# Kernel optimization log

Hardware: AMD Instinct MI355X
Metric: run time of the kernel (lower is better)

Reference implementation:

```python
import jax, jax.numpy as jnp
import numpy as np

N_NODES = 20000


def _gcn_norm(edge_index, n):
    src, dst = edge_index[0], edge_index[1]
    # degree of A + I (self-loops), all edge weights 1
    deg = jax.ops.segment_sum(jnp.ones(src.shape[0], jnp.float32), dst, num_segments=n) + 1.0
    dinv = jax.lax.rsqrt(deg)
    norm = dinv[src] * dinv[dst]          # [E]
    self_norm = dinv * dinv               # [N] self-loop coefficient = 1/deg
    return src, dst, norm, self_norm


def _gcn_layer(x, W, b, src, dst, norm, self_norm):
    # x: [B, N, Fin]; W: [Fin, Fout]
    h = jnp.einsum('bnf,fo->bno', x, W)   # transform first (PyG GCNConv order)
    msg = h[:, src, :] * norm[None, :, None]                      # [B, E, Fout]
    agg = jax.vmap(lambda m: jax.ops.segment_sum(m, dst, num_segments=x.shape[1]))(msg)
    agg = agg + h * self_norm[None, :, None]                      # self-loop term
    return agg + b


def setup_inputs() -> dict:
    key = jax.random.key(0)
    ks = jax.random.split(key, 8)
    B, N, Fin, H, O, E = 2, N_NODES, 256, 256, 64, 320000
    s = lambda f: 1.0 / np.sqrt(f)
    return {
        'x': jax.random.normal(ks[0], (B, N, Fin), jnp.float32),
        'W1': jax.random.normal(ks[1], (Fin, H), jnp.float32) * s(Fin),
        'b1': jnp.zeros((H,), jnp.float32),
        'W2': jax.random.normal(ks[2], (H, H), jnp.float32) * s(H),
        'b2': jnp.zeros((H,), jnp.float32),
        'Wfc': jax.random.normal(ks[3], (H, O), jnp.float32) * s(H),
        'bfc': jnp.zeros((O,), jnp.float32),
        'edge_index': jax.random.randint(ks[4], (2, E), 0, N, jnp.int64),
    }


def reference(x, W1, b1, W2, b2, Wfc, bfc, edge_index):
    src, dst, norm, self_norm = _gcn_norm(edge_index, x.shape[1])
    h = jax.nn.relu(_gcn_layer(x, W1, b1, src, dst, norm, self_norm))
    h = jax.nn.relu(_gcn_layer(h, W2, b2, src, dst, norm, self_norm))
    pooled = jnp.mean(h, axis=1)          # mean over nodes -> [B, H]
    return pooled @ Wfc + bfc             # [B, O]
```

## Files before the change

### kernel.cpp

```cpp
#include <hip/hip_runtime.h>

#define NNODES 20000
#define BATCH  2
#define FEAT   256
#define OOUT   64
#define PBLK   200
#define MROWS  40000
#define NPB    20096
#define H8ROWS 40192

typedef short  bhalf8 __attribute__((ext_vector_type(8)));
typedef float  floatx4 __attribute__((ext_vector_type(4)));
typedef float  floatx2 __attribute__((ext_vector_type(2)));

__device__ __forceinline__ float bf2f(unsigned short u) {
  return __uint_as_float(((unsigned int)u) << 16);
}
__device__ __forceinline__ unsigned short f2bf(float f) {
  unsigned int u = __float_as_uint(f);
  return (unsigned short)((u + 0x7fffu + ((u >> 16) & 1u)) >> 16);
}
__device__ __forceinline__ unsigned int pack4_fp8(float a, float b, float c, float d) {
  int p = __builtin_amdgcn_cvt_pk_fp8_f32(a, b, 0, false);
  p = __builtin_amdgcn_cvt_pk_fp8_f32(c, d, p, true);
  return (unsigned int)p;
}

__global__ __launch_bounds__(256) void prep_kernel(const float* __restrict__ W1,
                                                   const float* __restrict__ W2,
                                                   unsigned short* __restrict__ w1hi,
                                                   unsigned short* __restrict__ w1lo,
                                                   unsigned short* __restrict__ w2hi,
                                                   unsigned short* __restrict__ w2lo,
                                                   const int* __restrict__ raw, int E,
                                                   int* __restrict__ flag,
                                                   int* __restrict__ cnt,
                                                   int* __restrict__ fill) {
  int bid = blockIdx.x, tid = threadIdx.x;
  int idx = bid * 256 + tid;
  int which = idx >> 16, loc = idx & 65535;
  const float* W = which ? W2 : W1;
  unsigned short* Whi = which ? w2hi : w1hi;
  unsigned short* Wlo = which ? w2lo : w1lo;
  int k = loc >> 8, n = loc & 255;
  float w = W[loc];
  unsigned short hi = f2bf(w);
  unsigned short lo = f2bf(w - bf2f(hi));
  int g = n >> 4, ln = n & 15;
  int ks = k >> 5, ch = (k >> 3) & 3, j = k & 7;
  int addr = ((ks * 16 + g) * 64 + ch * 16 + ln) * 8 + j;
  Whi[addr] = hi;
  Wlo[addr] = lo;
  if (idx < NNODES) { cnt[idx] = 0; fill[idx] = 0; }
  if (bid == 511) {
    __shared__ int any;
    if (tid == 0) any = 0;
    __syncthreads();
    int nchk = E < 2048 ? E : 2048;
    for (int i = tid; i < nchk; i += 256)
      if (raw[2 * i + 1] != 0) any = 1;
    __syncthreads();
    if (tid == 0) *flag = any;
  }
}

__global__ void convert_count_kernel(const int* __restrict__ raw, const int* __restrict__ flag,
                                     int* __restrict__ s32, int* __restrict__ d32,
                                     int* __restrict__ cnt, int E) {
  int e = blockIdx.x * blockDim.x + threadIdx.x;
  if (e >= E) return;
  int s, d;
  if (*flag) { s = raw[e];     d = raw[E + e]; }
  else       { s = raw[2 * e]; d = raw[2 * (E + e)]; }
  s32[e] = s; d32[e] = d;
  atomicAdd(&cnt[d], 1);
}

__global__ __launch_bounds__(1024) void scan_dinv_kernel(const int* __restrict__ cnt,
                                                         int* __restrict__ row_start,
                                                         float* __restrict__ dinv, int n) {
  __shared__ int wsum[16];
  __shared__ int carry_s;
  int tid = threadIdx.x, lane = tid & 63, wv = tid >> 6;
  if (tid == 0) carry_s = 0;
  __syncthreads();
  for (int base = 0; base < n; base += 1024) {
    int v = (base + tid < n) ? cnt[base + tid] : 0;
    if (base + tid < n) dinv[base + tid] = 1.0f / sqrtf((float)(v + 1));
    int x = v;
#pragma unroll
    for (int off = 1; off < 64; off <<= 1) {
      int t = __shfl_up(x, off);
      if (lane >= off) x += t;
    }
    if (lane == 63) wsum[wv] = x;
    __syncthreads();
    int carry = carry_s;
    if (wv == 0) {
      int s = (lane < 16) ? wsum[lane] : 0;
#pragma unroll
      for (int off = 1; off < 16; off <<= 1) {
        int t = __shfl_up(s, off);
        if (lane >= off) s += t;
      }
      if (lane < 16) wsum[lane] = s;
    }
    __syncthreads();
    int woff = wv ? wsum[wv - 1] : 0;
    int total = wsum[15];
    if (base + tid < n) row_start[base + tid] = carry + woff + x - v;
    __syncthreads();
    if (tid == 0) carry_s = carry + total;
  }
  if (tid == 0) row_start[n] = carry_s;
}

__global__ void scatter_kernel(const int* __restrict__ s32, const int* __restrict__ d32,
                               const int* __restrict__ row_start, int* __restrict__ fill,
                               const float* __restrict__ dinv,
                               int* __restrict__ csr_src, float* __restrict__ csr_norm, int E) {
  int e = blockIdx.x * blockDim.x + threadIdx.x;
  if (e >= E) return;
  int s = s32[e], d = d32[e];
  int p = row_start[d] + atomicAdd(&fill[d], 1);
  csr_src[p] = s;
  csr_norm[p] = dinv[s] * dinv[d];
}

template <int AFP32>
__global__ __launch_bounds__(256) void gemm_mfma(const void* __restrict__ Av,
                                                 const unsigned short* __restrict__ Whi,
                                                 const unsigned short* __restrict__ Wlo,
                                                 unsigned int* __restrict__ C) {
  __shared__ unsigned short lds[2][8192];
  int bid = blockIdx.x;
  int tile = bid >> 1, half = bid & 1;
  int b = tile >= 157 ? 1 : 0;
  int nbase = (tile - b * 157) * 128;
  int tid = threadIdx.x, lane = tid & 63, wv = tid >> 6;
  int kc = (lane >> 4) * 8;

  const float* Af          = (const float*)Av;
  const unsigned short* Ab = (const unsigned short*)Av;

  int nn[2], mr[2];
#pragma unroll
  for (int t = 0; t < 2; ++t) {
    int nl = nbase + wv * 32 + t * 16 + (lane & 15);
    nn[t] = nl;
    int ncl = nl > NNODES - 1 ? NNODES - 1 : nl;
    mr[t] = b * NNODES + ncl;
  }

  floatx4 acc[2][8];
#pragma unroll
  for (int t = 0; t < 2; ++t)
#pragma unroll
    for (int g = 0; g < 8; ++g) acc[t][g] = (floatx4)(0.0f);

  bhalf8 st[4];
  auto stage_load = [&](int ks) {
#pragma unroll
    for (int i2 = 0; i2 < 4; ++i2) {
      int u = i2 * 256 + tid;
      int hl = u >> 9, g = (u >> 6) & 7, l = u & 63;
      const unsigned short* Wp = hl ? Wlo : Whi;
      st[i2] = *(const bhalf8*)&Wp[((size_t)(ks * 16 + half * 8 + g) * 64 + l) * 8];
    }
  };
  auto stage_write = [&](int buf) {
#pragma unroll
    for (int i2 = 0; i2 < 4; ++i2) {
      int u = i2 * 256 + tid;
      *(bhalf8*)&lds[buf][(size_t)u * 8] = st[i2];
    }
  };
  auto load_a = [&](int ks, bhalf8 (&a)[2]) {
#pragma unroll
    for (int t = 0; t < 2; ++t) {
      if (AFP32) {
        const float* p = &Af[(size_t)mr[t] * FEAT + ks * 32 + kc];
        float4 u = *(const float4*)p;
        float4 v = *(const float4*)(p + 4);
        a[t][0] = (short)f2bf(u.x); a[t][1] = (short)f2bf(u.y);
        a[t][2] = (short)f2bf(u.z); a[t][3] = (short)f2bf(u.w);
        a[t][4] = (short)f2bf(v.x); a[t][5] = (short)f2bf(v.y);
        a[t][6] = (short)f2bf(v.z); a[t][7] = (short)f2bf(v.w);
      } else {
        a[t] = *(const bhalf8*)&Ab[(size_t)mr[t] * FEAT + ks * 32 + kc];
      }
    }
  };
  auto step = [&](int buf, bhalf8 (&a)[2]) {
#pragma unroll
    for (int g = 0; g < 8; ++g) {
      bhalf8 bh = *(const bhalf8*)&lds[buf][((size_t)g * 64 + lane) * 8];
      bhalf8 bl = *(const bhalf8*)&lds[buf][((size_t)(512 + g * 64) + lane) * 8];
#pragma unroll
      for (int t = 0; t < 2; ++t)
        acc[t][g] = __builtin_amdgcn_mfma_f32_16x16x32_bf16(bh, a[t], acc[t][g], 0, 0, 0);
#pragma unroll
      for (int t = 0; t < 2; ++t)
        acc[t][g] = __builtin_amdgcn_mfma_f32_16x16x32_bf16(bl, a[t], acc[t][g], 0, 0, 0);
    }
  };

  stage_load(0);
  stage_write(0);
  __syncthreads();
  bhalf8 aC[2];
  load_a(0, aC);
  int cur = 0;
#pragma unroll
  for (int ks = 0; ks < 8; ++ks) {
    bhalf8 aN[2];
    if (ks < 7) {
      stage_load(ks + 1);
      load_a(ks + 1, aN);
    }
    step(cur, aC);
    if (ks < 7) {
      stage_write(cur ^ 1);
      __syncthreads();
      aC[0] = aN[0]; aC[1] = aN[1];
    }
    cur ^= 1;
  }

  int nc = (lane >> 4) * 4;
#pragma unroll
  for (int t = 0; t < 2; ++t) {
    size_t r = (size_t)nn[t] * 2 + b;
#pragma unroll
    for (int g = 0; g < 8; ++g) {
      int col = (half * 8 + g) * 16 + nc;
      C[r * 64 + (col >> 2)] =
          pack4_fp8(acc[t][g][0], acc[t][g][1], acc[t][g][2], acc[t][g][3]);
    }
  }
}

__global__ __launch_bounds__(128) void agg_kernel(const uint4* __restrict__ h8,
                                                  const int* __restrict__ row_start,
                                                  const int* __restrict__ csr_src,
                                                  const float* __restrict__ csr_norm,
                                                  const float* __restrict__ dinv,
                                                  const float* __restrict__ bias,
                                                  unsigned short* __restrict__ out) {
  int n = blockIdx.x;
  int tid = threadIdx.x;
  int wave = tid >> 6, lane = tid & 63;
  int q = (wave << 1) | (lane >> 5);
  int cl = lane & 31;

  float a[16];
#pragma unroll
  for (int j = 0; j < 16; ++j) a[j] = 0.0f;

  auto dec_fma = [&](uint4 m, float w) {
    unsigned int mm[4] = {m.x, m.y, m.z, m.w};
#pragma unroll
    for (int j = 0; j < 4; ++j) {
      floatx2 lo = __builtin_amdgcn_cvt_pk_f32_fp8((int)mm[j], false);
      floatx2 hi = __builtin_amdgcn_cvt_pk_f32_fp8((int)mm[j], true);
      a[j * 4 + 0] = fmaf(w, lo[0], a[j * 4 + 0]);
      a[j * 4 + 1] = fmaf(w, lo[1], a[j * 4 + 1]);
      a[j * 4 + 2] = fmaf(w, hi[0], a[j * 4 + 2]);
      a[j * 4 + 3] = fmaf(w, hi[1], a[j * 4 + 3]);
    }
  };

  float di = dinv[n];
  if (q == 0) dec_fma(h8[(size_t)n * 32 + cl], di * di);

  int s0 = row_start[n], s1 = row_start[n + 1];
  int i = s0 + q;
  for (; i + 4 < s1; i += 8) {
    int sa = csr_src[i], sb = csr_src[i + 4];
    float wa = csr_norm[i], wb = csr_norm[i + 4];
    uint4 ma = h8[(size_t)sa * 32 + cl];
    uint4 mb = h8[(size_t)sb * 32 + cl];
    dec_fma(ma, wa);
    dec_fma(mb, wb);
  }
  if (i < s1) dec_fma(h8[(size_t)csr_src[i] * 32 + cl], csr_norm[i]);

#pragma unroll
  for (int j = 0; j < 16; ++j) a[j] += __shfl_xor(a[j], 32);

  __shared__ float red[32][17];
  if (wave == 1 && lane < 32) {
#pragma unroll
    for (int j = 0; j < 16; ++j) red[lane][j] = a[j];
  }
  __syncthreads();
  if (wave == 0 && lane < 32) {
    int b = cl >> 4;
    int c = (cl & 15) * 16;
#pragma unroll
    for (int j = 0; j < 16; ++j) a[j] += red[lane][j];
    unsigned short o[16];
#pragma unroll
    for (int j = 0; j < 16; ++j)
      o[j] = f2bf(fmaxf(a[j] + bias[c + j], 0.0f));
    unsigned short* dst = &out[((size_t)b * NNODES + n) * FEAT + c];
    *(uint4*)dst = *(uint4*)&o[0];
    *(uint4*)(dst + 8) = *(uint4*)&o[8];
  }
}

__global__ __launch_bounds__(256) void pool_partial(const unsigned short* __restrict__ h2,
                                                    float* __restrict__ partials) {
  int blk = blockIdx.x;
  int c = threadIdx.x;
  int chunk = NNODES / PBLK;
  int n0 = blk * chunk;
  float s0 = 0.f, s1 = 0.f;
  for (int n = n0; n < n0 + chunk; ++n) {
    s0 += bf2f(h2[((size_t)0 * NNODES + n) * FEAT + c]);
    s1 += bf2f(h2[((size_t)1 * NNODES + n) * FEAT + c]);
  }
  partials[(blk * 2 + 0) * FEAT + c] = s0;
  partials[(blk * 2 + 1) * FEAT + c] = s1;
}

__global__ __launch_bounds__(256) void pool_fc(const float* __restrict__ partials,
                                               const float* __restrict__ Wfc, const float* __restrict__ bfc,
                                               float* __restrict__ out) {
  __shared__ float pooled[BATCH][FEAT];
  int t = threadIdx.x;
  float s0 = 0.f, s1 = 0.f;
  for (int p = 0; p < PBLK; ++p) {
    s0 += partials[(p * 2 + 0) * FEAT + t];
    s1 += partials[(p * 2 + 1) * FEAT + t];
  }
  pooled[0][t] = s0 / (float)NNODES;
  pooled[1][t] = s1 / (float)NNODES;
  __syncthreads();
  if (t < BATCH * OOUT) {
    int b = t >> 6, o = t & 63;
    float acc = bfc[o];
    for (int c2 = 0; c2 < FEAT; ++c2)
      acc = fmaf(pooled[b][c2], Wfc[c2 * OOUT + o], acc);
    out[b * OOUT + o] = acc;
  }
}

extern "C" void kernel_launch(void* const* d_in, const int* in_sizes, int n_in,
                              void* d_out, int out_size, void* d_ws, size_t ws_size,
                              hipStream_t stream) {
  const float* x    = (const float*)d_in[0];
  const float* W1   = (const float*)d_in[1];
  const float* b1   = (const float*)d_in[2];
  const float* W2   = (const float*)d_in[3];
  const float* b2   = (const float*)d_in[4];
  const float* Wfc  = (const float*)d_in[5];
  const float* bfc  = (const float*)d_in[6];
  const int*   eraw = (const int*)d_in[7];
  int E = in_sizes[7] / 2;
  float* out = (float*)d_out;

  char* ws = (char*)d_ws;
  size_t off = 0;
  auto alloc = [&](size_t elems4B) -> void* {
    void* p = ws + off * 4;
    off += (elems4B + 3) & ~(size_t)3;
    return p;
  };
  int*   flag      = (int*)alloc(4);
  int*   s32       = (int*)alloc(E);
  int*   d32       = (int*)alloc(E);
  int*   cnt       = (int*)alloc(NNODES);
  float* dinv      = (float*)alloc(NNODES);
  int*   row_start = (int*)alloc(NNODES + 1);
  int*   fill      = (int*)alloc(NNODES);
  int*   csr_src   = (int*)alloc(E);
  float* csr_norm  = (float*)alloc(E);
  unsigned short* w1hi = (unsigned short*)alloc(65536 / 2);
  unsigned short* w1lo = (unsigned short*)alloc(65536 / 2);
  unsigned short* w2hi = (unsigned short*)alloc(65536 / 2);
  unsigned short* w2lo = (unsigned short*)alloc(65536 / 2);
  unsigned int*   h8   = (unsigned int*)alloc((size_t)H8ROWS * 64);
  unsigned short* a1   = (unsigned short*)alloc((size_t)MROWS * FEAT / 2);
  float* partials  = (float*)alloc((size_t)PBLK * BATCH * FEAT);

  int eg = (E + 255) / 256;
  prep_kernel<<<512, 256, 0, stream>>>(W1, W2, w1hi, w1lo, w2hi, w2lo, eraw, E, flag, cnt, fill);
  convert_count_kernel<<<eg, 256, 0, stream>>>(eraw, flag, s32, d32, cnt, E);
  scan_dinv_kernel<<<1, 1024, 0, stream>>>(cnt, row_start, dinv, NNODES);
  scatter_kernel<<<eg, 256, 0, stream>>>(s32, d32, row_start, fill, dinv, csr_src, csr_norm, E);

  gemm_mfma<1><<<628, 256, 0, stream>>>(x, w1hi, w1lo, h8);
  agg_kernel<<<NNODES, 128, 0, stream>>>((const uint4*)h8, row_start, csr_src, csr_norm, dinv, b1, a1);
  gemm_mfma<0><<<628, 256, 0, stream>>>(a1, w2hi, w2lo, h8);
  agg_kernel<<<NNODES, 128, 0, stream>>>((const uint4*)h8, row_start, csr_src, csr_norm, dinv, b2, a1);
  pool_partial<<<PBLK, 256, 0, stream>>>(a1, partials);
  pool_fc<<<1, 256, 0, stream>>>(partials, Wfc, bfc, out);
}
```

Measured before the change: 188.9 us.

## Parallelize CSR scan, fuse layer-2 aggregation with pooling, remap GEMM blocks

Replaces the single-block serial scan with a 20-block chunked scan whose chunk offsets are added via atomics. It also drops the intermediate s32/d32 edge copies by re-reading the raw edge index in the scatter kernel. The second aggregation is fused with ReLU and mean pooling, so the layer-2 activations are never written out, and a 512-thread FC kernel reduces the per-block partials. The GEMM block index is remapped so both column halves of neighbouring tiles run close together, which should improve L2 reuse, at the cost of 12 idle padding blocks. The risk is a persistent-style agg2 loop with fewer blocks and two barriers per node.

```diff
diff --git a/kernel.cpp b/kernel.cpp
--- a/kernel.cpp
+++ b/kernel.cpp
@@ -4,10 +4,11 @@
 #define BATCH  2
 #define FEAT   256
 #define OOUT   64
-#define PBLK   200
 #define MROWS  40000
 #define NPB    20096
 #define H8ROWS 40192
+#define NCHUNK 20
+#define NB2    1280
 
 typedef short  bhalf8 __attribute__((ext_vector_type(8)));
 typedef float  floatx4 __attribute__((ext_vector_type(4)));
@@ -35,7 +36,8 @@
                                                    const int* __restrict__ raw, int E,
                                                    int* __restrict__ flag,
                                                    int* __restrict__ cnt,
-                                                   int* __restrict__ fill) {
+                                                   int* __restrict__ fill,
+                                                   int* __restrict__ chunkOff) {
   int bid = blockIdx.x, tid = threadIdx.x;
   int idx = bid * 256 + tid;
   int which = idx >> 16, loc = idx & 65535;
@@ -52,6 +54,7 @@
   Whi[addr] = hi;
   Wlo[addr] = lo;
   if (idx < NNODES) { cnt[idx] = 0; fill[idx] = 0; }
+  if (idx < NCHUNK) chunkOff[idx] = 0;
   if (bid == 511) {
     __shared__ int any;
     if (tid == 0) any = 0;
@@ -64,65 +67,61 @@
   }
 }
 
-__global__ void convert_count_kernel(const int* __restrict__ raw, const int* __restrict__ flag,
-                                     int* __restrict__ s32, int* __restrict__ d32,
-                                     int* __restrict__ cnt, int E) {
+__global__ void count_kernel(const int* __restrict__ raw, const int* __restrict__ flag,
+                             int* __restrict__ cnt, int E) {
+  int e = blockIdx.x * blockDim.x + threadIdx.x;
+  if (e >= E) return;
+  int d = (*flag) ? raw[E + e] : raw[2 * (E + e)];
+  atomicAdd(&cnt[d], 1);
+}
+
+__global__ __launch_bounds__(256) void scan_a_kernel(const int* __restrict__ cnt,
+                                                     int* __restrict__ row_start,
+                                                     float* __restrict__ dinv,
+                                                     int* __restrict__ chunkOff) {
+  int c = blockIdx.x, tid = threadIdx.x;
+  int base = c * 1024 + tid * 4;
+  int v[4]; int tsum = 0;
+#pragma unroll
+  for (int j = 0; j < 4; ++j) {
+    v[j] = (base + j < NNODES) ? cnt[base + j] : 0;
+    tsum += v[j];
+  }
+  int lane = tid & 63, wv = tid >> 6;
+  int x = tsum;
+#pragma unroll
+  for (int off = 1; off < 64; off <<= 1) {
+    int t = __shfl_up(x, off);
+    if (lane >= off) x += t;
+  }
+  __shared__ int wsum[4];
+  if (lane == 63) wsum[wv] = x;
+  __syncthreads();
+  int woff = 0;
+  for (int w = 0; w < wv; ++w) woff += wsum[w];
+  int run = woff + x - tsum;
+#pragma unroll
+  for (int j = 0; j < 4; ++j) {
+    if (base + j <= NNODES) row_start[base + j] = run;
+    if (base + j < NNODES) dinv[base + j] = 1.0f / sqrtf((float)(v[j] + 1));
+    run += v[j];
+  }
+  if (tid == 0) {
+    int T = wsum[0] + wsum[1] + wsum[2] + wsum[3];
+    for (int c2 = c + 1; c2 < NCHUNK; ++c2) atomicAdd(&chunkOff[c2], T);
+  }
+}
+
+__global__ void scatter_kernel(const int* __restrict__ raw, const int* __restrict__ flag,
+                               const int* __restrict__ row_start, const int* __restrict__ chunkOff,
+                               int* __restrict__ fill, const float* __restrict__ dinv,
+                               int* __restrict__ csr_src, float* __restrict__ csr_norm, int E) {
   int e = blockIdx.x * blockDim.x + threadIdx.x;
   if (e >= E) return;
   int s, d;
   if (*flag) { s = raw[e];     d = raw[E + e]; }
   else       { s = raw[2 * e]; d = raw[2 * (E + e)]; }
-  s32[e] = s; d32[e] = d;
-  atomicAdd(&cnt[d], 1);
-}
-
-__global__ __launch_bounds__(1024) void scan_dinv_kernel(const int* __restrict__ cnt,
-                                                         int* __restrict__ row_start,
-                                                         float* __restrict__ dinv, int n) {
-  __shared__ int wsum[16];
-  __shared__ int carry_s;
-  int tid = threadIdx.x, lane = tid & 63, wv = tid >> 6;
-  if (tid == 0) carry_s = 0;
-  __syncthreads();
-  for (int base = 0; base < n; base += 1024) {
-    int v = (base + tid < n) ? cnt[base + tid] : 0;
-    if (base + tid < n) dinv[base + tid] = 1.0f / sqrtf((float)(v + 1));
-    int x = v;
-#pragma unroll
-    for (int off = 1; off < 64; off <<= 1) {
-      int t = __shfl_up(x, off);
-      if (lane >= off) x += t;
-    }
-    if (lane == 63) wsum[wv] = x;
-    __syncthreads();
-    int carry = carry_s;
-    if (wv == 0) {
-      int s = (lane < 16) ? wsum[lane] : 0;
-#pragma unroll
-      for (int off = 1; off < 16; off <<= 1) {
-        int t = __shfl_up(s, off);
-        if (lane >= off) s += t;
-      }
-      if (lane < 16) wsum[lane] = s;
-    }
-    __syncthreads();
-    int woff = wv ? wsum[wv - 1] : 0;
-    int total = wsum[15];
-    if (base + tid < n) row_start[base + tid] = carry + woff + x - v;
-    __syncthreads();
-    if (tid == 0) carry_s = carry + total;
-  }
-  if (tid == 0) row_start[n] = carry_s;
-}
-
-__global__ void scatter_kernel(const int* __restrict__ s32, const int* __restrict__ d32,
-                               const int* __restrict__ row_start, int* __restrict__ fill,
-                               const float* __restrict__ dinv,
-                               int* __restrict__ csr_src, float* __restrict__ csr_norm, int E) {
-  int e = blockIdx.x * blockDim.x + threadIdx.x;
-  if (e >= E) return;
-  int s = s32[e], d = d32[e];
-  int p = row_start[d] + atomicAdd(&fill[d], 1);
+  int p = row_start[d] + chunkOff[d >> 10] + atomicAdd(&fill[d], 1);
   csr_src[p] = s;
   csr_norm[p] = dinv[s] * dinv[d];
 }
@@ -132,9 +131,11 @@
                                                  const unsigned short* __restrict__ Whi,
                                                  const unsigned short* __restrict__ Wlo,
                                                  unsigned int* __restrict__ C) {
+  int bid = blockIdx.x;
+  int tile = (bid >> 4) * 8 + (bid & 7);
+  int half = (bid >> 3) & 1;
+  if (tile >= 314) return;
   __shared__ unsigned short lds[2][8192];
-  int bid = blockIdx.x;
-  int tile = bid >> 1, half = bid & 1;
   int b = tile >= 157 ? 1 : 0;
   int nbase = (tile - b * 157) * 128;
   int tid = threadIdx.x, lane = tid & 63, wv = tid >> 6;
@@ -240,23 +241,14 @@
   }
 }
 
-__global__ __launch_bounds__(128) void agg_kernel(const uint4* __restrict__ h8,
-                                                  const int* __restrict__ row_start,
-                                                  const int* __restrict__ csr_src,
-                                                  const float* __restrict__ csr_norm,
-                                                  const float* __restrict__ dinv,
-                                                  const float* __restrict__ bias,
-                                                  unsigned short* __restrict__ out) {
-  int n = blockIdx.x;
-  int tid = threadIdx.x;
-  int wave = tid >> 6, lane = tid & 63;
-  int q = (wave << 1) | (lane >> 5);
-  int cl = lane & 31;
-
-  float a[16];
+struct AggCtx {
+  const uint4* h8; const int* row_start; const int* chunkOff;
+  const int* csr_src; const float* csr_norm; const float* dinv;
+};
+__device__ __forceinline__ void agg_compute(const AggCtx& g, int n, int q, int cl,
+                                            float (&a)[16]) {
 #pragma unroll
   for (int j = 0; j < 16; ++j) a[j] = 0.0f;
-
   auto dec_fma = [&](uint4 m, float w) {
     unsigned int mm[4] = {m.x, m.y, m.z, m.w};
 #pragma unroll
@@ -269,25 +261,31 @@
       a[j * 4 + 3] = fmaf(w, hi[1], a[j * 4 + 3]);
     }
   };
-
-  float di = dinv[n];
-  if (q == 0) dec_fma(h8[(size_t)n * 32 + cl], di * di);
-
-  int s0 = row_start[n], s1 = row_start[n + 1];
+  float di = g.dinv[n];
+  if (q == 0) dec_fma(g.h8[(size_t)n * 32 + cl], di * di);
+  int s0 = g.row_start[n] + g.chunkOff[n >> 10];
+  int s1 = g.row_start[n + 1] + g.chunkOff[(n + 1) >> 10];
   int i = s0 + q;
   for (; i + 4 < s1; i += 8) {
-    int sa = csr_src[i], sb = csr_src[i + 4];
-    float wa = csr_norm[i], wb = csr_norm[i + 4];
-    uint4 ma = h8[(size_t)sa * 32 + cl];
-    uint4 mb = h8[(size_t)sb * 32 + cl];
+    int sa = g.csr_src[i], sb = g.csr_src[i + 4];
+    float wa = g.csr_norm[i], wb = g.csr_norm[i + 4];
+    uint4 ma = g.h8[(size_t)sa * 32 + cl];
+    uint4 mb = g.h8[(size_t)sb * 32 + cl];
     dec_fma(ma, wa);
     dec_fma(mb, wb);
   }
-  if (i < s1) dec_fma(h8[(size_t)csr_src[i] * 32 + cl], csr_norm[i]);
-
+  if (i < s1) dec_fma(g.h8[(size_t)g.csr_src[i] * 32 + cl], g.csr_norm[i]);
 #pragma unroll
   for (int j = 0; j < 16; ++j) a[j] += __shfl_xor(a[j], 32);
-
+}
+
+__global__ __launch_bounds__(128) void agg1_kernel(AggCtx g, const float* __restrict__ bias,
+                                                   unsigned short* __restrict__ out) {
+  int n = blockIdx.x;
+  int tid = threadIdx.x, wave = tid >> 6, lane = tid & 63;
+  int q = (wave << 1) | (lane >> 5), cl = lane & 31;
+  float a[16];
+  agg_compute(g, n, q, cl, a);
   __shared__ float red[32][17];
   if (wave == 1 && lane < 32) {
 #pragma unroll
@@ -295,8 +293,7 @@
   }
   __syncthreads();
   if (wave == 0 && lane < 32) {
-    int b = cl >> 4;
-    int c = (cl & 15) * 16;
+    int b = cl >> 4, c = (cl & 15) * 16;
 #pragma unroll
     for (int j = 0; j < 16; ++j) a[j] += red[lane][j];
     unsigned short o[16];
@@ -309,39 +306,58 @@
   }
 }
 
-__global__ __launch_bounds__(256) void pool_partial(const unsigned short* __restrict__ h2,
-                                                    float* __restrict__ partials) {
-  int blk = blockIdx.x;
-  int c = threadIdx.x;
-  int chunk = NNODES / PBLK;
-  int n0 = blk * chunk;
-  float s0 = 0.f, s1 = 0.f;
-  for (int n = n0; n < n0 + chunk; ++n) {
-    s0 += bf2f(h2[((size_t)0 * NNODES + n) * FEAT + c]);
-    s1 += bf2f(h2[((size_t)1 * NNODES + n) * FEAT + c]);
-  }
-  partials[(blk * 2 + 0) * FEAT + c] = s0;
-  partials[(blk * 2 + 1) * FEAT + c] = s1;
-}
-
-__global__ __launch_bounds__(256) void pool_fc(const float* __restrict__ partials,
-                                               const float* __restrict__ Wfc, const float* __restrict__ bfc,
-                                               float* __restrict__ out) {
-  __shared__ float pooled[BATCH][FEAT];
+__global__ __launch_bounds__(128) void agg2pool_kernel(AggCtx g, const float* __restrict__ bias,
+                                                       float* __restrict__ partials) {
+  int bid = blockIdx.x;
+  int tid = threadIdx.x, wave = tid >> 6, lane = tid & 63;
+  int q = (wave << 1) | (lane >> 5), cl = lane & 31;
+  int b = cl >> 4, c = (cl & 15) * 16;
+  float pacc[16];
+#pragma unroll
+  for (int j = 0; j < 16; ++j) pacc[j] = 0.0f;
+  __shared__ float red[32][17];
+  for (int n = bid; n < NNODES; n += NB2) {
+    float a[16];
+    agg_compute(g, n, q, cl, a);
+    if (wave == 1 && lane < 32) {
+#pragma unroll
+      for (int j = 0; j < 16; ++j) red[lane][j] = a[j];
+    }
+    __syncthreads();
+    if (wave == 0 && lane < 32) {
+#pragma unroll
+      for (int j = 0; j < 16; ++j)
+        pacc[j] += fmaxf(a[j] + red[lane][j] + bias[c + j], 0.0f);
+    }
+    __syncthreads();
+  }
+  if (wave == 0 && lane < 32) {
+#pragma unroll
+    for (int j = 0; j < 16; ++j)
+      partials[(size_t)bid * 512 + b * 256 + c + j] = pacc[j];
+  }
+}
+
+__global__ __launch_bounds__(512) void fc_kernel(const float* __restrict__ partials,
+                                                 const float* __restrict__ Wfc,
+                                                 const float* __restrict__ bfc,
+                                                 float* __restrict__ out) {
+  __shared__ float pooled[512];
   int t = threadIdx.x;
-  float s0 = 0.f, s1 = 0.f;
-  for (int p = 0; p < PBLK; ++p) {
-    s0 += partials[(p * 2 + 0) * FEAT + t];
-    s1 += partials[(p * 2 + 1) * FEAT + t];
-  }
-  pooled[0][t] = s0 / (float)NNODES;
-  pooled[1][t] = s1 / (float)NNODES;
+  float s0 = 0.f, s1 = 0.f, s2 = 0.f, s3 = 0.f;
+  for (int p = 0; p < NB2; p += 4) {
+    s0 += partials[(size_t)(p + 0) * 512 + t];
+    s1 += partials[(size_t)(p + 1) * 512 + t];
+    s2 += partials[(size_t)(p + 2) * 512 + t];
+    s3 += partials[(size_t)(p + 3) * 512 + t];
+  }
+  pooled[t] = (s0 + s1 + s2 + s3) / (float)NNODES;
   __syncthreads();
   if (t < BATCH * OOUT) {
     int b = t >> 6, o = t & 63;
     float acc = bfc[o];
-    for (int c2 = 0; c2 < FEAT; ++c2)
-      acc = fmaf(pooled[b][c2], Wfc[c2 * OOUT + o], acc);
+    for (int f = 0; f < FEAT; ++f)
+      acc = fmaf(pooled[b * FEAT + f], Wfc[f * OOUT + o], acc);
     out[b * OOUT + o] = acc;
   }
 }
@@ -368,12 +384,11 @@
     return p;
   };
   int*   flag      = (int*)alloc(4);
-  int*   s32       = (int*)alloc(E);
-  int*   d32       = (int*)alloc(E);
   int*   cnt       = (int*)alloc(NNODES);
   float* dinv      = (float*)alloc(NNODES);
   int*   row_start = (int*)alloc(NNODES + 1);
   int*   fill      = (int*)alloc(NNODES);
+  int*   chunkOff  = (int*)alloc(NCHUNK + 4);
   int*   csr_src   = (int*)alloc(E);
   float* csr_norm  = (float*)alloc(E);
   unsigned short* w1hi = (unsigned short*)alloc(65536 / 2);
@@ -382,18 +397,23 @@
   unsigned short* w2lo = (unsigned short*)alloc(65536 / 2);
   unsigned int*   h8   = (unsigned int*)alloc((size_t)H8ROWS * 64);
   unsigned short* a1   = (unsigned short*)alloc((size_t)MROWS * FEAT / 2);
-  float* partials  = (float*)alloc((size_t)PBLK * BATCH * FEAT);
+  float* partials  = (float*)alloc((size_t)NB2 * 512);
 
   int eg = (E + 255) / 256;
-  prep_kernel<<<512, 256, 0, stream>>>(W1, W2, w1hi, w1lo, w2hi, w2lo, eraw, E, flag, cnt, fill);
-  convert_count_kernel<<<eg, 256, 0, stream>>>(eraw, flag, s32, d32, cnt, E);
-  scan_dinv_kernel<<<1, 1024, 0, stream>>>(cnt, row_start, dinv, NNODES);
-  scatter_kernel<<<eg, 256, 0, stream>>>(s32, d32, row_start, fill, dinv, csr_src, csr_norm, E);
-
-  gemm_mfma<1><<<628, 256, 0, stream>>>(x, w1hi, w1lo, h8);
-  agg_kernel<<<NNODES, 128, 0, stream>>>((const uint4*)h8, row_start, csr_src, csr_norm, dinv, b1, a1);
-  gemm_mfma<0><<<628, 256, 0, stream>>>(a1, w2hi, w2lo, h8);
-  agg_kernel<<<NNODES, 128, 0, stream>>>((const uint4*)h8, row_start, csr_src, csr_norm, dinv, b2, a1);
-  pool_partial<<<PBLK, 256, 0, stream>>>(a1, partials);
-  pool_fc<<<1, 256, 0, stream>>>(partials, Wfc, bfc, out);
-}
+  prep_kernel<<<512, 256, 0, stream>>>(W1, W2, w1hi, w1lo, w2hi, w2lo, eraw, E, flag,
+                                       cnt, fill, chunkOff);
+  count_kernel<<<eg, 256, 0, stream>>>(eraw, flag, cnt, E);
+  scan_a_kernel<<<NCHUNK, 256, 0, stream>>>(cnt, row_start, dinv, chunkOff);
+  scatter_kernel<<<eg, 256, 0, stream>>>(eraw, flag, row_start, chunkOff, fill, dinv,
+                                         csr_src, csr_norm, E);
+
+  AggCtx ag;
+  ag.h8 = (const uint4*)h8; ag.row_start = row_start; ag.chunkOff = chunkOff;
+  ag.csr_src = csr_src; ag.csr_norm = csr_norm; ag.dinv = dinv;
+
+  gemm_mfma<1><<<640, 256, 0, stream>>>(x, w1hi, w1lo, h8);
+  agg1_kernel<<<NNODES, 128, 0, stream>>>(ag, b1, a1);
+  gemm_mfma<0><<<640, 256, 0, stream>>>(a1, w2hi, w2lo, h8);
+  agg2pool_kernel<<<NB2, 128, 0, stream>>>(ag, b2, partials);
+  fc_kernel<<<1, 512, 0, stream>>>(partials, Wfc, bfc, out);
+}
```

Result: slower. 224.1 us (+18.6%).
